# Optimization experiments

Measured on AMD Instinct MI355X. Metric: run time of the kernel, lower is better.

## Reference

```python
import jax, jax.numpy as jnp
import numpy as np

DK = 128
B, S = 16, 2048

def setup_inputs() -> dict:
    key = jax.random.key(0)
    kq, kk, kv = jax.random.split(key, 3)
    q = jax.random.normal(kq, (B, S, DK), dtype=jnp.float32)
    k = jax.random.normal(kk, (B, S, DK), dtype=jnp.float32)
    v = jax.random.normal(kv, (B, S, DK), dtype=jnp.float32)
    return {"q": q, "k": k, "v": v}

def reference(q, k, v):
    # scores: [B, S, S]
    scale = 1.0 / jnp.sqrt(jnp.float32(DK))
    scores = jnp.einsum("bqd,bkd->bqk", q, k) * scale
    probs = jax.nn.softmax(scores, axis=-1)
    # dropout is identity in eval mode (training=None)
    return jnp.einsum("bqk,bkd->bqd", probs, v)
```

## Files before the change

kernel.cpp:

```cpp
#include <hip/hip_runtime.h>
#include <hip/hip_bf16.h>

#define BATCH 16
#define SEQ   2048
#define DK    128
#define NT    32
#define SC2   0.12751744f
#define THRL2 11.541560f

typedef __attribute__((ext_vector_type(8)))  short short8v;
typedef __attribute__((ext_vector_type(4)))  float float4v;
typedef __attribute__((ext_vector_type(16))) float float16v;

typedef const __attribute__((address_space(1))) unsigned int* gas_t;
typedef __attribute__((address_space(3))) unsigned int* las_t;

__device__ inline void gl_lds16(const void* g, void* l) {
    __builtin_amdgcn_global_load_lds((gas_t)g, (las_t)l, 16, 0, 0);
}

__device__ inline short f2bf(float f) {
    __hip_bfloat16 h = __float2bfloat16(f);
    unsigned short u;
    __builtin_memcpy(&u, &h, sizeof(u));
    return (short)u;
}

__device__ inline unsigned cvt_pk_bf16(float a, float b) {
    unsigned r;
    asm("v_cvt_pk_bf16_f32 %0, %1, %2" : "=v"(r) : "v"(a), "v"(b));
    return r;
}

__global__ __launch_bounds__(256)
void conv_k_kernel(const float* __restrict__ k, short* __restrict__ kb)
{
    size_t i = ((size_t)blockIdx.x * 256 + threadIdx.x) * 8;
    float4 a = *reinterpret_cast<const float4*>(k + i);
    float4 b = *reinterpret_cast<const float4*>(k + i + 4);
    short8v t;
    t[0] = f2bf(a.x * SC2); t[1] = f2bf(a.y * SC2); t[2] = f2bf(a.z * SC2); t[3] = f2bf(a.w * SC2);
    t[4] = f2bf(b.x * SC2); t[5] = f2bf(b.y * SC2); t[6] = f2bf(b.z * SC2); t[7] = f2bf(b.w * SC2);
    *reinterpret_cast<short8v*>(kb + i) = t;
}

__global__ __launch_bounds__(256)
void transpose_v_kernel(const float* __restrict__ v, short* __restrict__ vt)
{
    __shared__ float tile[32][33];
    const int tx = threadIdx.x & 31;
    const int ty = threadIdx.x >> 5;
    const int b  = blockIdx.z;
    const int s0 = blockIdx.x * 32;
    const int d0 = blockIdx.y * 32;

    const float* vb = v + ((size_t)b * SEQ + s0) * DK + d0;
#pragma unroll
    for (int i = 0; i < 4; ++i) {
        int r = ty + 8 * i;
        tile[r][tx] = vb[(size_t)r * DK + tx];
    }
    __syncthreads();

    const int s   = s0 + tx;
    const int kvl = s & 15;
    const int pos = (((kvl >> 2) & 1) << 3) | (((kvl >> 3) & 1) << 2) | (kvl & 3);
    const size_t col = (size_t)(s & ~15) | pos;

    short* vtb = vt + ((size_t)b * DK + d0) * SEQ;
#pragma unroll
    for (int i = 0; i < 4; ++i) {
        int r = ty + 8 * i;
        vtb[(size_t)r * SEQ + col] = f2bf(tile[tx][r]);
    }
}

__global__ __launch_bounds__(512, 2)
void attn_fwd_v8(const float* __restrict__ q,
                 const short* __restrict__ kb,
                 const short* __restrict__ vt,
                 float* __restrict__ out)
{
    __shared__ __align__(16) char lds[66560];

    const int tid  = threadIdx.x;
    const int lane = tid & 63;
    const int wave = tid >> 6;
    const int qt   = wave & 3;
    const int h    = wave >> 2;
    const int bid  = blockIdx.x;
    const int work = (bid & 7) * 32 + (bid >> 3);
    const int b    = work >> 4;
    const int q0   = (work & 15) * 128 + qt * 32;

    const int l31 = lane & 31;
    const int hi  = lane >> 5;

    const float* qrow = q + ((size_t)b * SEQ + q0 + l31) * DK + hi * 8;
    short8v qf[8];
#pragma unroll
    for (int s = 0; s < 8; ++s) {
        float4 x = *reinterpret_cast<const float4*>(qrow + s * 16);
        float4 y = *reinterpret_cast<const float4*>(qrow + s * 16 + 4);
        union { unsigned u[4]; short8v v; } pk;
        pk.u[0] = cvt_pk_bf16(x.x, x.y);
        pk.u[1] = cvt_pk_bf16(x.z, x.w);
        pk.u[2] = cvt_pk_bf16(y.x, y.y);
        pk.u[3] = cvt_pk_bf16(y.z, y.w);
        qf[s] = pk.v;
    }

    const char* kB = (const char*)(kb + (size_t)b * SEQ * DK);
    const char* vB = (const char*)(vt + (size_t)b * DK * SEQ);

    const char* src[4];
    int dstoff[4];
    long sstep;
    if (wave < 4) {
#pragma unroll
        for (int i = 0; i < 4; ++i) {
            const int c  = wave * 4 + i;
            const int hh = c >> 3, cc = c & 7;
            const int kr = cc * 4 + (lane >> 4);
            src[i] = kB + (size_t)(hh * 1024 + kr) * 256
                        + (((lane & 15) ^ (kr & 15)) << 4);
            dstoff[i] = hh * 16384 + cc * 1024;
        }
        sstep = 32 * 256;
    } else {
#pragma unroll
        for (int i = 0; i < 4; ++i) {
            const int c    = (wave - 4) * 4 + i;
            const int hh   = c >> 3, cc = c & 7;
            const int R    = cc * 8 + (lane >> 3);
            const int unit = (lane & 7) ^ (R & 7);
            const int d    = 2 * R + (unit >> 2);
            src[i] = vB + (size_t)d * (SEQ * 2) + hh * 2048 + (unit & 3) * 16;
            dstoff[i] = hh * 16384 + 8192 + cc * 1024;
        }
        sstep = 32 * 2;
    }

    float m_run = -1e30f;
    float l_run = 0.0f;
    float16v o[4];
#pragma unroll
    for (int dblk = 0; dblk < 4; ++dblk)
#pragma unroll
        for (int i = 0; i < 16; ++i) o[dblk][i] = 0.f;

    auto STAGE = [&](int bufsel, int t) {
        char* base = lds + bufsel * 32768;
#pragma unroll
        for (int i = 0; i < 4; ++i)
            gl_lds16(src[i] + (size_t)t * sstep, base + dstoff[i]);
    };

    STAGE(0, 0);
    __syncthreads();

    int buf = 0;
    for (int t = 0; t < NT; ++t) {
        if (t + 1 < NT) STAGE(buf ^ 1, t + 1);

        const char* Kl = lds + buf * 32768 + h * 16384;
        const char* Vl = Kl + 8192;
        const char* ka = Kl + l31 * 256;

        float16v sa;
#pragma unroll
        for (int i = 0; i < 16; ++i) sa[i] = 0.f;
        __builtin_amdgcn_s_setprio(1);
#pragma unroll
        for (int s = 0; s < 8; ++s) {
            const int un = ((2 * s + hi) ^ (l31 & 15)) << 4;
            short8v kf = *reinterpret_cast<const short8v*>(ka + un);
            sa = __builtin_amdgcn_mfma_f32_32x32x16_bf16(kf, qf[s], sa, 0, 0, 0);
        }
        __builtin_amdgcn_s_setprio(0);

        float mx = sa[0];
#pragma unroll
        for (int i = 1; i < 16; ++i) mx = fmaxf(mx, sa[i]);
        mx = fmaxf(mx, __shfl_xor(mx, 32));

        if (!__all(mx <= m_run + THRL2)) {
            const float mnew  = fmaxf(m_run, mx);
            const float alpha = exp2f(m_run - mnew);
            l_run *= alpha;
            m_run = mnew;
            float aq[16];
#pragma unroll
            for (int reg = 0; reg < 16; ++reg)
                aq[reg] = __shfl(alpha, (reg & 3) + 8 * (reg >> 2) + 4 * hi);
#pragma unroll
            for (int dblk = 0; dblk < 4; ++dblk)
#pragma unroll
                for (int reg = 0; reg < 16; ++reg) o[dblk][reg] *= aq[reg];
        }

        float ts = 0.f;
#pragma unroll
        for (int i = 0; i < 16; ++i) {
            const float e = exp2f(sa[i] - m_run);
            sa[i] = e;
            ts += e;
        }
        ts += __shfl_xor(ts, 32);
        l_run += ts;

        short8v pf[2];
#pragma unroll
        for (int g = 0; g < 2; ++g) {
            const int r0 = g * 8;
            union { unsigned u[4]; short8v v; } pk;
            pk.u[0] = cvt_pk_bf16(sa[r0 + 0], sa[r0 + 1]);
            pk.u[1] = cvt_pk_bf16(sa[r0 + 2], sa[r0 + 3]);
            pk.u[2] = cvt_pk_bf16(sa[r0 + 4], sa[r0 + 5]);
            pk.u[3] = cvt_pk_bf16(sa[r0 + 6], sa[r0 + 7]);
            pf[g] = pk.v;
        }

        __builtin_amdgcn_s_setprio(1);
#pragma unroll
        for (int dblk = 0; dblk < 4; ++dblk) {
            const int R  = dblk * 16 + (l31 >> 1);
            const char* vr = Vl + R * 128;
            const int dh4 = (l31 & 1) << 2;
#pragma unroll
            for (int g = 0; g < 2; ++g) {
                const int w = ((dh4 | (2 * g + hi)) ^ (R & 7)) << 4;
                short8v vf = *reinterpret_cast<const short8v*>(vr + w);
                o[dblk] = __builtin_amdgcn_mfma_f32_32x32x16_bf16(pf[g], vf, o[dblk], 0, 0, 0);
            }
        }
        __builtin_amdgcn_s_setprio(0);

        __syncthreads();
        buf ^= 1;
    }

    float* smO = (float*)lds;
    float* smM = (float*)(lds + 65536);
    float* smL = (float*)(lds + 66048);

    if (h == 1) {
        if (hi == 0) { smM[qt * 32 + l31] = m_run; smL[qt * 32 + l31] = l_run; }
#pragma unroll
        for (int dblk = 0; dblk < 4; ++dblk)
#pragma unroll
            for (int reg = 0; reg < 16; ++reg) {
                const int qp = (reg & 3) + 8 * (reg >> 2) + 4 * hi;
                smO[(qt * 32 + qp) * 128 + dblk * 32 + l31] = o[dblk][reg];
            }
    }
    __syncthreads();
    if (h == 0) {
        const float m1 = smM[qt * 32 + l31];
        const float l1 = smL[qt * 32 + l31];
        const float mf = fmaxf(m_run, m1);
        const float a0 = exp2f(m_run - mf);
        const float a1 = exp2f(m1 - mf);
        const float li = 1.0f / (l_run * a0 + l1 * a1);
        const float w0 = a0 * li;
        const float w1 = a1 * li;

        float w0q[16], w1q[16];
#pragma unroll
        for (int reg = 0; reg < 16; ++reg) {
            const int qp = (reg & 3) + 8 * (reg >> 2) + 4 * hi;
            w0q[reg] = __shfl(w0, qp);
            w1q[reg] = __shfl(w1, qp);
        }

        float* ob = out + ((size_t)b * SEQ + q0) * DK;
#pragma unroll
        for (int dblk = 0; dblk < 4; ++dblk)
#pragma unroll
            for (int reg = 0; reg < 16; ++reg) {
                const int qp = (reg & 3) + 8 * (reg >> 2) + 4 * hi;
                ob[(size_t)qp * DK + dblk * 32 + l31] =
                    o[dblk][reg] * w0q[reg]
                    + smO[(qt * 32 + qp) * 128 + dblk * 32 + l31] * w1q[reg];
            }
    }
}

__global__ __launch_bounds__(256)
void attn_fwd_slow(const float* __restrict__ q,
                   const float* __restrict__ k,
                   const float* __restrict__ v,
                   float* __restrict__ out)
{
    const int lane = threadIdx.x & 63;
    const int wave = threadIdx.x >> 6;
    const int b    = blockIdx.y;
    const int q0   = blockIdx.x * 64 + wave * 16;
    const int row = lane & 15;
    const int grp = lane >> 4;

    const float* qb = q + ((size_t)b * SEQ + q0) * DK;
    const float* kbp = k + (size_t)b * SEQ * DK;
    const float* vbp = v + (size_t)b * SEQ * DK;

    short8v qf[4];
#pragma unroll
    for (int c = 0; c < 4; ++c) {
        const float* p = qb + row * DK + c * 32 + grp * 8;
        float4 x = *reinterpret_cast<const float4*>(p);
        float4 y = *reinterpret_cast<const float4*>(p + 4);
        short8v t;
        t[0] = f2bf(x.x); t[1] = f2bf(x.y); t[2] = f2bf(x.z); t[3] = f2bf(x.w);
        t[4] = f2bf(y.x); t[5] = f2bf(y.y); t[6] = f2bf(y.z); t[7] = f2bf(y.w);
        qf[c] = t;
    }

    float m_run = -1e30f, l_run = 0.0f;
    float4v o[8];
#pragma unroll
    for (int i = 0; i < 8; ++i) { o[i][0]=0.f; o[i][1]=0.f; o[i][2]=0.f; o[i][3]=0.f; }
    const float scale = 0.08838834764831845f;

    for (int kv0 = 0; kv0 < SEQ; kv0 += 16) {
        short8v kf[4];
        const float* kp0 = kbp + (size_t)(kv0 + row) * DK + grp * 8;
#pragma unroll
        for (int c = 0; c < 4; ++c) {
            const float* p = kp0 + c * 32;
            float4 x = *reinterpret_cast<const float4*>(p);
            float4 y = *reinterpret_cast<const float4*>(p + 4);
            short8v t;
            t[0] = f2bf(x.x); t[1] = f2bf(x.y); t[2] = f2bf(x.z); t[3] = f2bf(x.w);
            t[4] = f2bf(y.x); t[5] = f2bf(y.y); t[6] = f2bf(y.z); t[7] = f2bf(y.w);
            kf[c] = t;
        }
        short8v vf[8];
#pragma unroll
        for (int dblk = 0; dblk < 8; ++dblk) {
            const float* p = vbp + (size_t)(kv0 + 4 * grp) * DK + dblk * 16 + row;
            short b0 = f2bf(p[0]);
            short b1 = f2bf(p[DK]);
            short b2 = f2bf(p[2 * DK]);
            short b3 = f2bf(p[3 * DK]);
            short8v t;
            t[0]=b0; t[1]=b1; t[2]=b2; t[3]=b3; t[4]=b0; t[5]=b1; t[6]=b2; t[7]=b3;
            vf[dblk] = t;
        }
        float4v s; s[0]=0.f; s[1]=0.f; s[2]=0.f; s[3]=0.f;
#pragma unroll
        for (int c = 0; c < 4; ++c)
            s = __builtin_amdgcn_mfma_f32_16x16x32_bf16(kf[c], qf[c], s, 0, 0, 0);

        float sv[4]; float tmax = -1e30f;
#pragma unroll
        for (int r = 0; r < 4; ++r) { sv[r] = s[r] * scale; tmax = fmaxf(tmax, sv[r]); }
        tmax = fmaxf(tmax, __shfl_xor(tmax, 16));
        tmax = fmaxf(tmax, __shfl_xor(tmax, 32));
        const float mnew = fmaxf(m_run, tmax);
        float pr[4]; float tsum = 0.f;
#pragma unroll
        for (int r = 0; r < 4; ++r) { pr[r] = __expf(sv[r] - mnew); tsum += pr[r]; }
        tsum += __shfl_xor(tsum, 16);
        tsum += __shfl_xor(tsum, 32);
        const float alpha = __expf(m_run - mnew);
        l_run = l_run * alpha + tsum;
        m_run = mnew;
        float aq[4];
#pragma unroll
        for (int r = 0; r < 4; ++r) aq[r] = __shfl(alpha, grp * 4 + r);
#pragma unroll
        for (int dblk = 0; dblk < 8; ++dblk)
#pragma unroll
            for (int r = 0; r < 4; ++r) o[dblk][r] *= aq[r];

        short8v pfv;
        pfv[0]=f2bf(pr[0]); pfv[1]=f2bf(pr[1]); pfv[2]=f2bf(pr[2]); pfv[3]=f2bf(pr[3]);
        pfv[4]=0; pfv[5]=0; pfv[6]=0; pfv[7]=0;
#pragma unroll
        for (int dblk = 0; dblk < 8; ++dblk)
            o[dblk] = __builtin_amdgcn_mfma_f32_16x16x32_bf16(pfv, vf[dblk], o[dblk], 0, 0, 0);
    }

    const float linv = 1.0f / l_run;
    float li[4];
#pragma unroll
    for (int r = 0; r < 4; ++r) li[r] = __shfl(linv, grp * 4 + r);
    float* ob = out + ((size_t)b * SEQ + q0) * DK;
#pragma unroll
    for (int dblk = 0; dblk < 8; ++dblk)
#pragma unroll
        for (int r = 0; r < 4; ++r)
            ob[(size_t)(grp * 4 + r) * DK + dblk * 16 + row] = o[dblk][r] * li[r];
}

extern "C" void kernel_launch(void* const* d_in, const int* in_sizes, int n_in,
                              void* d_out, int out_size, void* d_ws, size_t ws_size,
                              hipStream_t stream) {
    const float* q = (const float*)d_in[0];
    const float* k = (const float*)d_in[1];
    const float* v = (const float*)d_in[2];
    float* out = (float*)d_out;

    const size_t kb_bytes = (size_t)BATCH * SEQ * DK * sizeof(short);
    const size_t need = 2 * kb_bytes;

    if (ws_size >= need) {
        short* kb = (short*)d_ws;
        short* vt = (short*)((char*)d_ws + kb_bytes);
        hipLaunchKernelGGL(conv_k_kernel, dim3(2048), dim3(256), 0, stream, k, kb);
        hipLaunchKernelGGL(transpose_v_kernel, dim3(SEQ / 32, DK / 32, BATCH), dim3(256), 0, stream, v, vt);
        hipLaunchKernelGGL(attn_fwd_v8, dim3((SEQ / 128) * BATCH), dim3(512), 0, stream, q, kb, vt, out);
    } else {
        hipLaunchKernelGGL(attn_fwd_slow, dim3(SEQ / 64, BATCH), dim3(256), 0, stream, q, k, v, out);
    }
}
```

Baseline: 70.75 us.

## Prefetch two tiles ahead with explicit vmcnt waits and raw barriers

Restructures the K/V tile loop so two tiles are in flight before compute starts. Each iteration waits only for the older tile's global-to-LDS loads (vmcnt(4)), computes, then syncs and refills the buffer just consumed with tile t+2. The goal is to hide global load latency better than the previous single-prefetch loop, which relied on __syncthreads. The cost is hand-written waitcnt and sched barriers that depend on the exact count of outstanding loads per stage.

```diff
diff --git a/kernel.cpp b/kernel.cpp
--- a/kernel.cpp
+++ b/kernel.cpp
@@ -76,7 +76,7 @@
 }
 
 __global__ __launch_bounds__(512, 2)
-void attn_fwd_v8(const float* __restrict__ q,
+void attn_fwd_v9(const float* __restrict__ q,
                  const short* __restrict__ kb,
                  const short* __restrict__ vt,
                  float* __restrict__ out)
@@ -156,14 +156,8 @@
             gl_lds16(src[i] + (size_t)t * sstep, base + dstoff[i]);
     };
 
-    STAGE(0, 0);
-    __syncthreads();
-
-    int buf = 0;
-    for (int t = 0; t < NT; ++t) {
-        if (t + 1 < NT) STAGE(buf ^ 1, t + 1);
-
-        const char* Kl = lds + buf * 32768 + h * 16384;
+    auto COMPUTE = [&](int bufsel) {
+        const char* Kl = lds + bufsel * 32768 + h * 16384;
         const char* Vl = Kl + 8192;
         const char* ka = Kl + l31 * 256;
 
@@ -235,10 +229,39 @@
             }
         }
         __builtin_amdgcn_s_setprio(0);
-
-        __syncthreads();
+    };
+
+    STAGE(0, 0);
+    STAGE(1, 1);
+
+    int buf = 0;
+    for (int t = 0; t < NT - 1; ++t) {
+        asm volatile("s_waitcnt vmcnt(4)" ::: "memory");
+        __builtin_amdgcn_sched_barrier(0);
+        __builtin_amdgcn_s_barrier();
+        __builtin_amdgcn_sched_barrier(0);
+
+        COMPUTE(buf);
+
+        asm volatile("s_waitcnt lgkmcnt(0)" ::: "memory");
+        __builtin_amdgcn_sched_barrier(0);
+        __builtin_amdgcn_s_barrier();
+        __builtin_amdgcn_sched_barrier(0);
+
+        if (t < NT - 2) STAGE(buf, t + 2);
         buf ^= 1;
     }
+    asm volatile("s_waitcnt vmcnt(0)" ::: "memory");
+    __builtin_amdgcn_sched_barrier(0);
+    __builtin_amdgcn_s_barrier();
+    __builtin_amdgcn_sched_barrier(0);
+
+    COMPUTE(buf);
+
+    asm volatile("s_waitcnt lgkmcnt(0)" ::: "memory");
+    __builtin_amdgcn_sched_barrier(0);
+    __builtin_amdgcn_s_barrier();
+    __builtin_amdgcn_sched_barrier(0);
 
     float* smO = (float*)lds;
     float* smM = (float*)(lds + 65536);
@@ -409,7 +432,7 @@
         short* vt = (short*)((char*)d_ws + kb_bytes);
         hipLaunchKernelGGL(conv_k_kernel, dim3(2048), dim3(256), 0, stream, k, kb);
         hipLaunchKernelGGL(transpose_v_kernel, dim3(SEQ / 32, DK / 32, BATCH), dim3(256), 0, stream, v, vt);
-        hipLaunchKernelGGL(attn_fwd_v8, dim3((SEQ / 128) * BATCH), dim3(512), 0, stream, q, kb, vt, out);
+        hipLaunchKernelGGL(attn_fwd_v9, dim3((SEQ / 128) * BATCH), dim3(512), 0, stream, q, kb, vt, out);
     } else {
         hipLaunchKernelGGL(attn_fwd_slow, dim3(SEQ / 64, BATCH), dim3(256), 0, stream, q, k, v, out);
     }
```

Result: slower. 72.24 us (+2.1%).

## Give each wave two query tiles and split KV four ways with tree merge

Applied to the files above, without the earlier changes.

Each wave now computes two 32-row query tiles so every K and V fragment read from LDS feeds two MFMAs, halving LDS read traffic per flop. Waves are reorganized into 2 query groups by 4 KV-partitions with 16 iterations each, and partial softmax states are combined via a two-level LDS merge. This doubles the LDS footprint and accumulator register use, risking spills and lower occupancy.

```diff
diff --git a/kernel.cpp b/kernel.cpp
--- a/kernel.cpp
+++ b/kernel.cpp
@@ -4,7 +4,7 @@
 #define BATCH 16
 #define SEQ   2048
 #define DK    128
-#define NT    32
+#define NT    16
 #define SC2   0.12751744f
 #define THRL2 11.541560f
 
@@ -76,84 +76,82 @@
 }
 
 __global__ __launch_bounds__(512, 2)
-void attn_fwd_v8(const float* __restrict__ q,
-                 const short* __restrict__ kb,
-                 const short* __restrict__ vt,
-                 float* __restrict__ out)
+void attn_fwd_v10(const float* __restrict__ q,
+                  const short* __restrict__ kb,
+                  const short* __restrict__ vt,
+                  float* __restrict__ out)
 {
-    __shared__ __align__(16) char lds[66560];
+    __shared__ __align__(16) char lds[133120];
 
     const int tid  = threadIdx.x;
     const int lane = tid & 63;
     const int wave = tid >> 6;
-    const int qt   = wave & 3;
-    const int h    = wave >> 2;
+    const int qw   = wave & 1;
+    const int h    = wave >> 1;
     const int bid  = blockIdx.x;
     const int work = (bid & 7) * 32 + (bid >> 3);
     const int b    = work >> 4;
-    const int q0   = (work & 15) * 128 + qt * 32;
+    const int q0   = (work & 15) * 128 + qw * 64;
 
     const int l31 = lane & 31;
     const int hi  = lane >> 5;
 
-    const float* qrow = q + ((size_t)b * SEQ + q0 + l31) * DK + hi * 8;
-    short8v qf[8];
-#pragma unroll
-    for (int s = 0; s < 8; ++s) {
-        float4 x = *reinterpret_cast<const float4*>(qrow + s * 16);
-        float4 y = *reinterpret_cast<const float4*>(qrow + s * 16 + 4);
-        union { unsigned u[4]; short8v v; } pk;
-        pk.u[0] = cvt_pk_bf16(x.x, x.y);
-        pk.u[1] = cvt_pk_bf16(x.z, x.w);
-        pk.u[2] = cvt_pk_bf16(y.x, y.y);
-        pk.u[3] = cvt_pk_bf16(y.z, y.w);
-        qf[s] = pk.v;
+    short8v qf0[8], qf1[8];
+    {
+        const float* qr0 = q + ((size_t)b * SEQ + q0 + l31) * DK + hi * 8;
+        const float* qr1 = qr0 + 32 * DK;
+#pragma unroll
+        for (int s = 0; s < 8; ++s) {
+            float4 x = *reinterpret_cast<const float4*>(qr0 + s * 16);
+            float4 y = *reinterpret_cast<const float4*>(qr0 + s * 16 + 4);
+            union { unsigned u[4]; short8v v; } pk;
+            pk.u[0] = cvt_pk_bf16(x.x, x.y);
+            pk.u[1] = cvt_pk_bf16(x.z, x.w);
+            pk.u[2] = cvt_pk_bf16(y.x, y.y);
+            pk.u[3] = cvt_pk_bf16(y.z, y.w);
+            qf0[s] = pk.v;
+            x = *reinterpret_cast<const float4*>(qr1 + s * 16);
+            y = *reinterpret_cast<const float4*>(qr1 + s * 16 + 4);
+            pk.u[0] = cvt_pk_bf16(x.x, x.y);
+            pk.u[1] = cvt_pk_bf16(x.z, x.w);
+            pk.u[2] = cvt_pk_bf16(y.x, y.y);
+            pk.u[3] = cvt_pk_bf16(y.z, y.w);
+            qf1[s] = pk.v;
+        }
     }
 
     const char* kB = (const char*)(kb + (size_t)b * SEQ * DK);
     const char* vB = (const char*)(vt + (size_t)b * DK * SEQ);
 
-    const char* src[4];
-    int dstoff[4];
-    long sstep;
-    if (wave < 4) {
-#pragma unroll
-        for (int i = 0; i < 4; ++i) {
-            const int c  = wave * 4 + i;
-            const int hh = c >> 3, cc = c & 7;
-            const int kr = cc * 4 + (lane >> 4);
-            src[i] = kB + (size_t)(hh * 1024 + kr) * 256
-                        + (((lane & 15) ^ (kr & 15)) << 4);
-            dstoff[i] = hh * 16384 + cc * 1024;
-        }
-        sstep = 32 * 256;
-    } else {
-#pragma unroll
-        for (int i = 0; i < 4; ++i) {
-            const int c    = (wave - 4) * 4 + i;
-            const int hh   = c >> 3, cc = c & 7;
-            const int R    = cc * 8 + (lane >> 3);
-            const int unit = (lane & 7) ^ (R & 7);
-            const int d    = 2 * R + (unit >> 2);
-            src[i] = vB + (size_t)d * (SEQ * 2) + hh * 2048 + (unit & 3) * 16;
-            dstoff[i] = hh * 16384 + 8192 + cc * 1024;
-        }
-        sstep = 32 * 2;
-    }
-
-    float m_run = -1e30f;
-    float l_run = 0.0f;
-    float16v o[4];
+    float mA = -1e30f, lA = 0.0f;
+    float mB = -1e30f, lB = 0.0f;
+    float16v o0[4], o1[4];
 #pragma unroll
     for (int dblk = 0; dblk < 4; ++dblk)
 #pragma unroll
-        for (int i = 0; i < 16; ++i) o[dblk][i] = 0.f;
+        for (int i = 0; i < 16; ++i) { o0[dblk][i] = 0.f; o1[dblk][i] = 0.f; }
 
     auto STAGE = [&](int bufsel, int t) {
-        char* base = lds + bufsel * 32768;
-#pragma unroll
-        for (int i = 0; i < 4; ++i)
-            gl_lds16(src[i] + (size_t)t * sstep, base + dstoff[i]);
+        char* base = lds + bufsel * 65536 + h * 16384;
+        if (qw == 0) {
+            const char* ksrc = kB + (size_t)(h * 512 + t * 32) * 256;
+#pragma unroll
+            for (int i = 0; i < 8; ++i) {
+                const int kr = i * 4 + (lane >> 4);
+                gl_lds16(ksrc + (size_t)kr * 256
+                              + (((lane & 15) ^ ((i & 3) << 2) ^ (lane >> 4)) << 4),
+                         base + i * 1024);
+            }
+        } else {
+            const char* vsrc = vB + (size_t)h * 1024 + (size_t)t * 64;
+            const int unit = (lane & 7) ^ (lane >> 3);
+#pragma unroll
+            for (int i = 0; i < 8; ++i) {
+                const int d = 16 * i + 2 * (lane >> 3) + (unit >> 2);
+                gl_lds16(vsrc + (size_t)d * 4096 + (unit & 3) * 16,
+                         base + 8192 + i * 1024);
+            }
+        }
     };
 
     STAGE(0, 0);
@@ -163,62 +161,97 @@
     for (int t = 0; t < NT; ++t) {
         if (t + 1 < NT) STAGE(buf ^ 1, t + 1);
 
-        const char* Kl = lds + buf * 32768 + h * 16384;
+        const char* Kl = lds + buf * 65536 + h * 16384;
         const char* Vl = Kl + 8192;
         const char* ka = Kl + l31 * 256;
 
-        float16v sa;
-#pragma unroll
-        for (int i = 0; i < 16; ++i) sa[i] = 0.f;
+        float16v sa0, sa1;
+#pragma unroll
+        for (int i = 0; i < 16; ++i) { sa0[i] = 0.f; sa1[i] = 0.f; }
         __builtin_amdgcn_s_setprio(1);
 #pragma unroll
         for (int s = 0; s < 8; ++s) {
             const int un = ((2 * s + hi) ^ (l31 & 15)) << 4;
             short8v kf = *reinterpret_cast<const short8v*>(ka + un);
-            sa = __builtin_amdgcn_mfma_f32_32x32x16_bf16(kf, qf[s], sa, 0, 0, 0);
+            sa0 = __builtin_amdgcn_mfma_f32_32x32x16_bf16(kf, qf0[s], sa0, 0, 0, 0);
+            sa1 = __builtin_amdgcn_mfma_f32_32x32x16_bf16(kf, qf1[s], sa1, 0, 0, 0);
         }
         __builtin_amdgcn_s_setprio(0);
 
-        float mx = sa[0];
-#pragma unroll
-        for (int i = 1; i < 16; ++i) mx = fmaxf(mx, sa[i]);
-        mx = fmaxf(mx, __shfl_xor(mx, 32));
-
-        if (!__all(mx <= m_run + THRL2)) {
-            const float mnew  = fmaxf(m_run, mx);
-            const float alpha = exp2f(m_run - mnew);
-            l_run *= alpha;
-            m_run = mnew;
-            float aq[16];
-#pragma unroll
-            for (int reg = 0; reg < 16; ++reg)
-                aq[reg] = __shfl(alpha, (reg & 3) + 8 * (reg >> 2) + 4 * hi);
-#pragma unroll
-            for (int dblk = 0; dblk < 4; ++dblk)
-#pragma unroll
-                for (int reg = 0; reg < 16; ++reg) o[dblk][reg] *= aq[reg];
-        }
-
-        float ts = 0.f;
-#pragma unroll
-        for (int i = 0; i < 16; ++i) {
-            const float e = exp2f(sa[i] - m_run);
-            sa[i] = e;
-            ts += e;
-        }
-        ts += __shfl_xor(ts, 32);
-        l_run += ts;
-
-        short8v pf[2];
+        {
+            float mx = sa0[0];
+#pragma unroll
+            for (int i = 1; i < 16; ++i) mx = fmaxf(mx, sa0[i]);
+            mx = fmaxf(mx, __shfl_xor(mx, 32));
+            if (!__all(mx <= mA + THRL2)) {
+                const float mnew  = fmaxf(mA, mx);
+                const float alpha = exp2f(mA - mnew);
+                lA *= alpha;
+                mA = mnew;
+                float aq[16];
+#pragma unroll
+                for (int reg = 0; reg < 16; ++reg)
+                    aq[reg] = __shfl(alpha, (reg & 3) + 8 * (reg >> 2) + 4 * hi);
+#pragma unroll
+                for (int dblk = 0; dblk < 4; ++dblk)
+#pragma unroll
+                    for (int reg = 0; reg < 16; ++reg) o0[dblk][reg] *= aq[reg];
+            }
+            float ts = 0.f;
+#pragma unroll
+            for (int i = 0; i < 16; ++i) {
+                const float e = exp2f(sa0[i] - mA);
+                sa0[i] = e;
+                ts += e;
+            }
+            ts += __shfl_xor(ts, 32);
+            lA += ts;
+        }
+        {
+            float mx = sa1[0];
+#pragma unroll
+            for (int i = 1; i < 16; ++i) mx = fmaxf(mx, sa1[i]);
+            mx = fmaxf(mx, __shfl_xor(mx, 32));
+            if (!__all(mx <= mB + THRL2)) {
+                const float mnew  = fmaxf(mB, mx);
+                const float alpha = exp2f(mB - mnew);
+                lB *= alpha;
+                mB = mnew;
+                float aq[16];
+#pragma unroll
+                for (int reg = 0; reg < 16; ++reg)
+                    aq[reg] = __shfl(alpha, (reg & 3) + 8 * (reg >> 2) + 4 * hi);
+#pragma unroll
+                for (int dblk = 0; dblk < 4; ++dblk)
+#pragma unroll
+                    for (int reg = 0; reg < 16; ++reg) o1[dblk][reg] *= aq[reg];
+            }
+            float ts = 0.f;
+#pragma unroll
+            for (int i = 0; i < 16; ++i) {
+                const float e = exp2f(sa1[i] - mB);
+                sa1[i] = e;
+                ts += e;
+            }
+            ts += __shfl_xor(ts, 32);
+            lB += ts;
+        }
+
+        short8v pf0[2], pf1[2];
 #pragma unroll
         for (int g = 0; g < 2; ++g) {
             const int r0 = g * 8;
             union { unsigned u[4]; short8v v; } pk;
-            pk.u[0] = cvt_pk_bf16(sa[r0 + 0], sa[r0 + 1]);
-            pk.u[1] = cvt_pk_bf16(sa[r0 + 2], sa[r0 + 3]);
-            pk.u[2] = cvt_pk_bf16(sa[r0 + 4], sa[r0 + 5]);
-            pk.u[3] = cvt_pk_bf16(sa[r0 + 6], sa[r0 + 7]);
-            pf[g] = pk.v;
+            pk.u[0] = cvt_pk_bf16(sa0[r0 + 0], sa0[r0 + 1]);
+            pk.u[1] = cvt_pk_bf16(sa0[r0 + 2], sa0[r0 + 3]);
+            pk.u[2] = cvt_pk_bf16(sa0[r0 + 4], sa0[r0 + 5]);
+            pk.u[3] = cvt_pk_bf16(sa0[r0 + 6], sa0[r0 + 7]);
+            pf0[g] = pk.v;
+            pk.u[0] = cvt_pk_bf16(sa1[r0 + 0], sa1[r0 + 1]);
+            pk.u[1] = cvt_pk_bf16(sa1[r0 + 2], sa1[r0 + 3]);
+            pk.u[2] = cvt_pk_bf16(sa1[r0 + 4], sa1[r0 + 5]);
+            pk.u[3] = cvt_pk_bf16(sa1[r0 + 6], sa1[r0 + 7]);
+            pf1[g] = pk.v;
         }
 
         __builtin_amdgcn_s_setprio(1);
@@ -231,7 +264,8 @@
             for (int g = 0; g < 2; ++g) {
                 const int w = ((dh4 | (2 * g + hi)) ^ (R & 7)) << 4;
                 short8v vf = *reinterpret_cast<const short8v*>(vr + w);
-                o[dblk] = __builtin_amdgcn_mfma_f32_32x32x16_bf16(pf[g], vf, o[dblk], 0, 0, 0);
+                o0[dblk] = __builtin_amdgcn_mfma_f32_32x32x16_bf16(pf0[g], vf, o0[dblk], 0, 0, 0);
+                o1[dblk] = __builtin_amdgcn_mfma_f32_32x32x16_bf16(pf1[g], vf, o1[dblk], 0, 0, 0);
             }
         }
         __builtin_amdgcn_s_setprio(0);
@@ -240,48 +274,103 @@
         buf ^= 1;
     }
 
-    float* smO = (float*)lds;
-    float* smM = (float*)(lds + 65536);
-    float* smL = (float*)(lds + 66048);
-
-    if (h == 1) {
-        if (hi == 0) { smM[qt * 32 + l31] = m_run; smL[qt * 32 + l31] = l_run; }
+    auto WRITE_REGION = [&](int rid) {
+        float* ro = (float*)(lds + rid * 32768);
+        float* ml = (float*)(lds + 131072) + rid * 128;
 #pragma unroll
         for (int dblk = 0; dblk < 4; ++dblk)
 #pragma unroll
             for (int reg = 0; reg < 16; ++reg) {
                 const int qp = (reg & 3) + 8 * (reg >> 2) + 4 * hi;
-                smO[(qt * 32 + qp) * 128 + dblk * 32 + l31] = o[dblk][reg];
-            }
-    }
+                ro[(qp) * 128 + dblk * 32 + l31]      = o0[dblk][reg];
+                ro[(32 + qp) * 128 + dblk * 32 + l31] = o1[dblk][reg];
+            }
+        if (hi == 0) {
+            ml[l31 * 2]          = mA;
+            ml[l31 * 2 + 1]      = lA;
+            ml[64 + l31 * 2]     = mB;
+            ml[64 + l31 * 2 + 1] = lB;
+        }
+    };
+
+    auto MERGE_FROM = [&](int rid) {
+        float* ro = (float*)(lds + rid * 32768);
+        float* ml = (float*)(lds + 131072) + rid * 128;
+        {
+            const float m1 = ml[l31 * 2];
+            const float l1 = ml[l31 * 2 + 1];
+            const float mf = fmaxf(mA, m1);
+            const float a0 = exp2f(mA - mf);
+            const float a1 = exp2f(m1 - mf);
+            lA = lA * a0 + l1 * a1;
+            mA = mf;
+            float a0q[16], a1q[16];
+#pragma unroll
+            for (int reg = 0; reg < 16; ++reg) {
+                const int qp = (reg & 3) + 8 * (reg >> 2) + 4 * hi;
+                a0q[reg] = __shfl(a0, qp);
+                a1q[reg] = __shfl(a1, qp);
+            }
+#pragma unroll
+            for (int dblk = 0; dblk < 4; ++dblk)
+#pragma unroll
+                for (int reg = 0; reg < 16; ++reg) {
+                    const int qp = (reg & 3) + 8 * (reg >> 2) + 4 * hi;
+                    o0[dblk][reg] = o0[dblk][reg] * a0q[reg]
+                                  + ro[qp * 128 + dblk * 32 + l31] * a1q[reg];
+                }
+        }
+        {
+            const float m1 = ml[64 + l31 * 2];
+            const float l1 = ml[64 + l31 * 2 + 1];
+            const float mf = fmaxf(mB, m1);
+            const float a0 = exp2f(mB - mf);
+            const float a1 = exp2f(m1 - mf);
+            lB = lB * a0 + l1 * a1;
+            mB = mf;
+            float a0q[16], a1q[16];
+#pragma unroll
+            for (int reg = 0; reg < 16; ++reg) {
+                const int qp = (reg & 3) + 8 * (reg >> 2) + 4 * hi;
+                a0q[reg] = __shfl(a0, qp);
+                a1q[reg] = __shfl(a1, qp);
+            }
+#pragma unroll
+            for (int dblk = 0; dblk < 4; ++dblk)
+#pragma unroll
+                for (int reg = 0; reg < 16; ++reg) {
+                    const int qp = (reg & 3) + 8 * (reg >> 2) + 4 * hi;
+                    o1[dblk][reg] = o1[dblk][reg] * a0q[reg]
+                                  + ro[(32 + qp) * 128 + dblk * 32 + l31] * a1q[reg];
+                }
+        }
+    };
+
+    if (h == 1 || h == 3) WRITE_REGION((h >> 1) * 2 + qw);
+    __syncthreads();
+    if (h == 0 || h == 2) MERGE_FROM((h >> 1) * 2 + qw);
+    __syncthreads();
+    if (h == 2) WRITE_REGION(qw);
     __syncthreads();
     if (h == 0) {
-        const float m1 = smM[qt * 32 + l31];
-        const float l1 = smL[qt * 32 + l31];
-        const float mf = fmaxf(m_run, m1);
-        const float a0 = exp2f(m_run - mf);
-        const float a1 = exp2f(m1 - mf);
-        const float li = 1.0f / (l_run * a0 + l1 * a1);
-        const float w0 = a0 * li;
-        const float w1 = a1 * li;
-
-        float w0q[16], w1q[16];
+        MERGE_FROM(qw);
+        const float liA = 1.0f / lA;
+        const float liB = 1.0f / lB;
+        float lAq[16], lBq[16];
 #pragma unroll
         for (int reg = 0; reg < 16; ++reg) {
             const int qp = (reg & 3) + 8 * (reg >> 2) + 4 * hi;
-            w0q[reg] = __shfl(w0, qp);
-            w1q[reg] = __shfl(w1, qp);
-        }
-
+            lAq[reg] = __shfl(liA, qp);
+            lBq[reg] = __shfl(liB, qp);
+        }
         float* ob = out + ((size_t)b * SEQ + q0) * DK;
 #pragma unroll
         for (int dblk = 0; dblk < 4; ++dblk)
 #pragma unroll
             for (int reg = 0; reg < 16; ++reg) {
                 const int qp = (reg & 3) + 8 * (reg >> 2) + 4 * hi;
-                ob[(size_t)qp * DK + dblk * 32 + l31] =
-                    o[dblk][reg] * w0q[reg]
-                    + smO[(qt * 32 + qp) * 128 + dblk * 32 + l31] * w1q[reg];
+                ob[(size_t)qp * DK + dblk * 32 + l31]        = o0[dblk][reg] * lAq[reg];
+                ob[(size_t)(32 + qp) * DK + dblk * 32 + l31] = o1[dblk][reg] * lBq[reg];
             }
     }
 }
@@ -409,7 +498,7 @@
         short* vt = (short*)((char*)d_ws + kb_bytes);
         hipLaunchKernelGGL(conv_k_kernel, dim3(2048), dim3(256), 0, stream, k, kb);
         hipLaunchKernelGGL(transpose_v_kernel, dim3(SEQ / 32, DK / 32, BATCH), dim3(256), 0, stream, v, vt);
-        hipLaunchKernelGGL(attn_fwd_v8, dim3((SEQ / 128) * BATCH), dim3(512), 0, stream, q, kb, vt, out);
+        hipLaunchKernelGGL(attn_fwd_v10, dim3((SEQ / 128) * BATCH), dim3(512), 0, stream, q, kb, vt, out);
     } else {
         hipLaunchKernelGGL(attn_fwd_slow, dim3(SEQ / 64, BATCH), dim3(256), 0, stream, q, k, v, out);
     }
```

Result: slower. 98.20 us (+38.8%).

## Split KV sequence four ways across 16 waves with tree merge of partial outputs

Applied to the files above, without the earlier changes.

The attention kernel moves from 8 to 16 waves per block (1024 threads). The key/value sequence is split into four segments instead of two, so each wave runs half as many KV tiles. Partial softmax states are combined by a two-level reduction through LDS with extra barriers, and normalisation happens once at the end. The aim is more in-flight waves per block and a shorter per-wave loop. In exchange it doubles LDS per block to about 130KB, which allows only one block per CU, increases register pressure under the 1024-thread launch bound, and adds merge work.

```diff
diff --git a/kernel.cpp b/kernel.cpp
--- a/kernel.cpp
+++ b/kernel.cpp
@@ -4,7 +4,7 @@
 #define BATCH 16
 #define SEQ   2048
 #define DK    128
-#define NT    32
+#define NT    16
 #define SC2   0.12751744f
 #define THRL2 11.541560f
 
@@ -75,13 +75,13 @@
     }
 }
 
-__global__ __launch_bounds__(512, 2)
-void attn_fwd_v8(const float* __restrict__ q,
-                 const short* __restrict__ kb,
-                 const short* __restrict__ vt,
-                 float* __restrict__ out)
+__global__ __launch_bounds__(1024)
+void attn_fwd_v11(const float* __restrict__ q,
+                  const short* __restrict__ kb,
+                  const short* __restrict__ vt,
+                  float* __restrict__ out)
 {
-    __shared__ __align__(16) char lds[66560];
+    __shared__ __align__(16) char lds[133120];
 
     const int tid  = threadIdx.x;
     const int lane = tid & 63;
@@ -116,27 +116,27 @@
     const char* src[4];
     int dstoff[4];
     long sstep;
-    if (wave < 4) {
+    if (wave < 8) {
+        const int seg = wave >> 1, p = wave & 1;
 #pragma unroll
         for (int i = 0; i < 4; ++i) {
-            const int c  = wave * 4 + i;
-            const int hh = c >> 3, cc = c & 7;
+            const int cc = p * 4 + i;
             const int kr = cc * 4 + (lane >> 4);
-            src[i] = kB + (size_t)(hh * 1024 + kr) * 256
+            src[i] = kB + (size_t)(seg * 512 + kr) * 256
                         + (((lane & 15) ^ (kr & 15)) << 4);
-            dstoff[i] = hh * 16384 + cc * 1024;
+            dstoff[i] = seg * 16384 + cc * 1024;
         }
         sstep = 32 * 256;
     } else {
+        const int seg = (wave - 8) >> 1, p = wave & 1;
 #pragma unroll
         for (int i = 0; i < 4; ++i) {
-            const int c    = (wave - 4) * 4 + i;
-            const int hh   = c >> 3, cc = c & 7;
+            const int cc   = p * 4 + i;
             const int R    = cc * 8 + (lane >> 3);
             const int unit = (lane & 7) ^ (R & 7);
             const int d    = 2 * R + (unit >> 2);
-            src[i] = vB + (size_t)d * (SEQ * 2) + hh * 2048 + (unit & 3) * 16;
-            dstoff[i] = hh * 16384 + 8192 + cc * 1024;
+            src[i] = vB + (size_t)d * 4096 + seg * 1024 + (unit & 3) * 16;
+            dstoff[i] = seg * 16384 + 8192 + cc * 1024;
         }
         sstep = 32 * 2;
     }
@@ -150,7 +150,7 @@
         for (int i = 0; i < 16; ++i) o[dblk][i] = 0.f;
 
     auto STAGE = [&](int bufsel, int t) {
-        char* base = lds + bufsel * 32768;
+        char* base = lds + bufsel * 65536;
 #pragma unroll
         for (int i = 0; i < 4; ++i)
             gl_lds16(src[i] + (size_t)t * sstep, base + dstoff[i]);
@@ -163,7 +163,7 @@
     for (int t = 0; t < NT; ++t) {
         if (t + 1 < NT) STAGE(buf ^ 1, t + 1);
 
-        const char* Kl = lds + buf * 32768 + h * 16384;
+        const char* Kl = lds + buf * 65536 + h * 16384;
         const char* Vl = Kl + 8192;
         const char* ka = Kl + l31 * 256;
 
@@ -240,48 +240,71 @@
         buf ^= 1;
     }
 
-    float* smO = (float*)lds;
-    float* smM = (float*)(lds + 65536);
-    float* smL = (float*)(lds + 66048);
-
-    if (h == 1) {
-        if (hi == 0) { smM[qt * 32 + l31] = m_run; smL[qt * 32 + l31] = l_run; }
+    auto WRITE_REGION = [&](int rid) {
+        float* ro = (float*)(lds + rid * 16384);
+        float* ml = (float*)(lds + 131072) + rid * 64;
 #pragma unroll
         for (int dblk = 0; dblk < 4; ++dblk)
 #pragma unroll
             for (int reg = 0; reg < 16; ++reg) {
                 const int qp = (reg & 3) + 8 * (reg >> 2) + 4 * hi;
-                smO[(qt * 32 + qp) * 128 + dblk * 32 + l31] = o[dblk][reg];
+                ro[qp * 128 + dblk * 32 + l31] = o[dblk][reg];
             }
-    }
-    __syncthreads();
-    if (h == 0) {
-        const float m1 = smM[qt * 32 + l31];
-        const float l1 = smL[qt * 32 + l31];
+        if (hi == 0) {
+            ml[l31 * 2]     = m_run;
+            ml[l31 * 2 + 1] = l_run;
+        }
+    };
+
+    auto MERGE_FROM = [&](int rid) {
+        float* ro = (float*)(lds + rid * 16384);
+        float* ml = (float*)(lds + 131072) + rid * 64;
+        const float m1 = ml[l31 * 2];
+        const float l1 = ml[l31 * 2 + 1];
         const float mf = fmaxf(m_run, m1);
         const float a0 = exp2f(m_run - mf);
         const float a1 = exp2f(m1 - mf);
-        const float li = 1.0f / (l_run * a0 + l1 * a1);
-        const float w0 = a0 * li;
-        const float w1 = a1 * li;
-
-        float w0q[16], w1q[16];
+        l_run = l_run * a0 + l1 * a1;
+        m_run = mf;
+        float a0q[16], a1q[16];
 #pragma unroll
         for (int reg = 0; reg < 16; ++reg) {
             const int qp = (reg & 3) + 8 * (reg >> 2) + 4 * hi;
-            w0q[reg] = __shfl(w0, qp);
-            w1q[reg] = __shfl(w1, qp);
-        }
-
-        float* ob = out + ((size_t)b * SEQ + q0) * DK;
+            a0q[reg] = __shfl(a0, qp);
+            a1q[reg] = __shfl(a1, qp);
+        }
 #pragma unroll
         for (int dblk = 0; dblk < 4; ++dblk)
 #pragma unroll
             for (int reg = 0; reg < 16; ++reg) {
                 const int qp = (reg & 3) + 8 * (reg >> 2) + 4 * hi;
-                ob[(size_t)qp * DK + dblk * 32 + l31] =
-                    o[dblk][reg] * w0q[reg]
-                    + smO[(qt * 32 + qp) * 128 + dblk * 32 + l31] * w1q[reg];
+                o[dblk][reg] = o[dblk][reg] * a0q[reg]
+                             + ro[qp * 128 + dblk * 32 + l31] * a1q[reg];
+            }
+    };
+
+    if (h == 1 || h == 3) WRITE_REGION(qt + 4 * (h >> 1));
+    __syncthreads();
+    if (h == 0 || h == 2) MERGE_FROM(qt + 4 * (h >> 1));
+    __syncthreads();
+    if (h == 2) WRITE_REGION(qt);
+    __syncthreads();
+    if (h == 0) {
+        MERGE_FROM(qt);
+        const float li = 1.0f / l_run;
+        float liq[16];
+#pragma unroll
+        for (int reg = 0; reg < 16; ++reg) {
+            const int qp = (reg & 3) + 8 * (reg >> 2) + 4 * hi;
+            liq[reg] = __shfl(li, qp);
+        }
+        float* ob = out + ((size_t)b * SEQ + q0) * DK;
+#pragma unroll
+        for (int dblk = 0; dblk < 4; ++dblk)
+#pragma unroll
+            for (int reg = 0; reg < 16; ++reg) {
+                const int qp = (reg & 3) + 8 * (reg >> 2) + 4 * hi;
+                ob[(size_t)qp * DK + dblk * 32 + l31] = o[dblk][reg] * liq[reg];
             }
     }
 }
@@ -409,7 +432,7 @@
         short* vt = (short*)((char*)d_ws + kb_bytes);
         hipLaunchKernelGGL(conv_k_kernel, dim3(2048), dim3(256), 0, stream, k, kb);
         hipLaunchKernelGGL(transpose_v_kernel, dim3(SEQ / 32, DK / 32, BATCH), dim3(256), 0, stream, v, vt);
-        hipLaunchKernelGGL(attn_fwd_v8, dim3((SEQ / 128) * BATCH), dim3(512), 0, stream, q, kb, vt, out);
+        hipLaunchKernelGGL(attn_fwd_v11, dim3((SEQ / 128) * BATCH), dim3(1024), 0, stream, q, kb, vt, out);
     } else {
         hipLaunchKernelGGL(attn_fwd_slow, dim3(SEQ / 64, BATCH), dim3(256), 0, stream, q, k, v, out);
     }
```

New measurement: 140.4 us. 1.99x slower.
